# Performance work log

Measured on AMD Instinct MI355X. Metric: run time of the kernel, lower is better.

## Reference

```python
import jax, jax.numpy as jnp
import numpy as np

VOCAB = 10000
HIDDEN = 256
BATCH = 32
SEQ = 256


def setup_inputs() -> dict:
    key = jax.random.key(0)
    ks = jax.random.split(key, 7)
    s = 1.0 / np.sqrt(HIDDEN)  # torch nn.RNN/Linear init scale
    return {
        "inputs": jax.random.randint(ks[0], (BATCH, SEQ), 0, VOCAB),
        "state": jnp.zeros((1, BATCH, HIDDEN), dtype=jnp.float32),
        "W_ih": jax.random.uniform(ks[1], (HIDDEN, VOCAB), jnp.float32, -s, s),
        "b_ih": jax.random.uniform(ks[2], (HIDDEN,), jnp.float32, -s, s),
        "W_hh": jax.random.uniform(ks[3], (HIDDEN, HIDDEN), jnp.float32, -s, s),
        "b_hh": jax.random.uniform(ks[4], (HIDDEN,), jnp.float32, -s, s),
        "W_out": jax.random.uniform(ks[5], (VOCAB, HIDDEN), jnp.float32, -s, s),
        "b_out": jax.random.uniform(ks[6], (VOCAB,), jnp.float32, -s, s),
    }


def reference(inputs, state, W_ih, b_ih, W_hh, b_hh, W_out, b_out):
    # one_hot(inputs.T) @ W_ih.T is exactly a row-gather of W_ih.T (one-hot
    # entries are exactly 1.0), so gather gives bitwise-identical math.
    # xproj: (seq, batch, hidden)
    xproj = W_ih.T[inputs.T] + b_ih + b_hh

    def step(h, x_t):
        h = jnp.tanh(x_t + h @ W_hh.T)  # (batch, hidden)
        return h, h

    h_last, Y = jax.lax.scan(step, state[0], xproj)  # Y: (seq, batch, hidden)
    logits = Y.reshape(-1, HIDDEN) @ W_out.T + b_out  # (seq*batch, vocab)
    return logits, h_last[None]
```

## Files before the change

kernel.cpp:

```cpp
#include <hip/hip_runtime.h>

#define VOCAB 10000
#define HIDDEN 256
#define BATCH 32
#define SEQ 256
#define M_ROWS 8192
#define NPAD 10112
#define NTILES 79
#define MTILES 64
#define LOGITS_ELEMS 81920000LL

typedef __attribute__((ext_vector_type(8))) short short8;
typedef __attribute__((ext_vector_type(4))) float f32x4;

static __device__ __forceinline__ unsigned short f32_to_bf16(float f) {
    unsigned u = __float_as_uint(f);
    u += 0x7fffu + ((u >> 16) & 1u);
    return (unsigned short)(u >> 16);
}

__global__ __launch_bounds__(256) void transpose_wih(const float* __restrict__ W_ih,
                                                     float* __restrict__ W_ihT) {
    __shared__ float tile[64][65];
    const int v0   = (blockIdx.x >> 2) * 64;
    const int h0   = (blockIdx.x & 3) * 64;
    const int lane = threadIdx.x & 63;
    const int wv   = threadIdx.x >> 6;

#pragma unroll
    for (int i = 0; i < 16; ++i) {
        const int row = i * 4 + wv;
        const int v   = v0 + lane;
        if (v < VOCAB)
            tile[row][lane] = W_ih[(long)(h0 + row) * VOCAB + v];
    }
    __syncthreads();
#pragma unroll
    for (int i = 0; i < 16; ++i) {
        const int vrow = i * 4 + wv;
        const int v    = v0 + vrow;
        if (v < VOCAB)
            W_ihT[(long)v * HIDDEN + h0 + lane] = tile[lane][vrow];
    }
}

__global__ __launch_bounds__(256) void prep_wout(const float* __restrict__ W_out,
                                                 unsigned short* __restrict__ Wb) {
    const int n = blockIdx.x;
    const int k = threadIdx.x;
    float v = (n < VOCAB) ? W_out[(long)n * HIDDEN + k] : 0.f;
    Wb[(long)n * HIDDEN + k] = f32_to_bf16(v);
}

__global__ __launch_bounds__(512, 2) void scan_kernel(
        const int*   __restrict__ inputs,
        const float* __restrict__ state,
        const float* __restrict__ W_hh,
        const float* __restrict__ b_ih,
        const float* __restrict__ b_hh,
        const float* __restrict__ W_ihT,
        unsigned short* __restrict__ Ybf,
        float* __restrict__ hout)
{
    __shared__ float hbuf[HIDDEN];
    __shared__ float psum[4 * HIDDEN];

    const int b  = blockIdx.x;
    const int t  = threadIdx.x;
    const int jj = t & 63;
    const int q  = (t >> 6) & 3;
    const int h2 = t >> 8;

    float w[2][64];
#pragma unroll
    for (int r = 0; r < 2; ++r) {
        const float* src = W_hh + (jj + 64 * (2 * h2 + r)) * HIDDEN + 64 * q;
#pragma unroll
        for (int k4 = 0; k4 < 16; ++k4) {
            const float4 v = *(const float4*)(src + 4 * k4);
            w[r][4 * k4 + 0] = v.x;
            w[r][4 * k4 + 1] = v.y;
            w[r][4 * k4 + 2] = v.z;
            w[r][4 * k4 + 3] = v.w;
        }
    }

    float biasv = 0.f, xcur = 0.f;
    if (t < HIDDEN) {
        biasv   = b_ih[t] + b_hh[t];
        hbuf[t] = state[b * HIDDEN + t];
        const int tok0 = inputs[b * SEQ];
        xcur = W_ihT[(long)tok0 * HIDDEN + t];
    }
    __syncthreads();

    for (int step = 0; step < SEQ; ++step) {
        float xnext = 0.f;
        if (t < HIDDEN && step + 1 < SEQ) {
            const int tokn = inputs[b * SEQ + step + 1];
            xnext = W_ihT[(long)tokn * HIDDEN + t];
        }

        float a00 = 0.f, a01 = 0.f, a10 = 0.f, a11 = 0.f;
#pragma unroll
        for (int k4 = 0; k4 < 8; ++k4) {
            const float4 hv = *(const float4*)&hbuf[64 * q + 4 * k4];
            a00 = fmaf(w[0][4 * k4 + 0], hv.x, a00);
            a00 = fmaf(w[0][4 * k4 + 1], hv.y, a00);
            a00 = fmaf(w[0][4 * k4 + 2], hv.z, a00);
            a00 = fmaf(w[0][4 * k4 + 3], hv.w, a00);
            a10 = fmaf(w[1][4 * k4 + 0], hv.x, a10);
            a10 = fmaf(w[1][4 * k4 + 1], hv.y, a10);
            a10 = fmaf(w[1][4 * k4 + 2], hv.z, a10);
            a10 = fmaf(w[1][4 * k4 + 3], hv.w, a10);
        }
#pragma unroll
        for (int k4 = 8; k4 < 16; ++k4) {
            const float4 hv = *(const float4*)&hbuf[64 * q + 4 * k4];
            a01 = fmaf(w[0][4 * k4 + 0], hv.x, a01);
            a01 = fmaf(w[0][4 * k4 + 1], hv.y, a01);
            a01 = fmaf(w[0][4 * k4 + 2], hv.z, a01);
            a01 = fmaf(w[0][4 * k4 + 3], hv.w, a01);
            a11 = fmaf(w[1][4 * k4 + 0], hv.x, a11);
            a11 = fmaf(w[1][4 * k4 + 1], hv.y, a11);
            a11 = fmaf(w[1][4 * k4 + 2], hv.z, a11);
            a11 = fmaf(w[1][4 * k4 + 3], hv.w, a11);
        }
        psum[q * HIDDEN + jj + 64 * (2 * h2 + 0)] = a00 + a01;
        psum[q * HIDDEN + jj + 64 * (2 * h2 + 1)] = a10 + a11;
        __syncthreads();

        if (t < HIDDEN) {
            const float s = psum[t] + psum[HIDDEN + t]
                          + psum[2 * HIDDEN + t] + psum[3 * HIDDEN + t];
            const float hnew = tanhf(s + xcur + biasv);
            hbuf[t] = hnew;
            Ybf[((long)step * BATCH + b) * HIDDEN + t] = f32_to_bf16(hnew);
            xcur = xnext;
        }
        __syncthreads();
    }

    if (t < HIDDEN) hout[b * HIDDEN + t] = hbuf[t];
}

__global__ __launch_bounds__(256) void gemm_kernel(
        const unsigned short* __restrict__ A,
        const unsigned short* __restrict__ B,
        const float* __restrict__ bias,
        float* __restrict__ C)
{
    __shared__ unsigned short lA[128 * 64];
    __shared__ unsigned short lB[128 * 64];

    const int t     = threadIdx.x;
    const int bid   = blockIdx.x;
    const int ntile = bid % NTILES;
    const int mtile = bid / NTILES;
    const long m0   = (long)mtile * 128;
    const long n0   = (long)ntile * 128;
    const int lane  = t & 63;
    const int wave  = t >> 6;
    const int wm    = (wave & 1) * 64;
    const int wn    = (wave >> 1) * 64;
    const int l15   = lane & 15;
    const int quad  = lane >> 4;

    const f32x4 zero = {0.f, 0.f, 0.f, 0.f};
    f32x4 acc[4][4];
#pragma unroll
    for (int i = 0; i < 4; ++i)
#pragma unroll
        for (int j = 0; j < 4; ++j)
            acc[i][j] = zero;

    for (int kb = 0; kb < 4; ++kb) {
        if (kb) __syncthreads();
#pragma unroll
        for (int it = 0; it < 4; ++it) {
            const int c   = it * 256 + t;
            const int row = c >> 3;
            const int k8  = c & 7;
            const unsigned short* ga = A + (m0 + row) * HIDDEN + kb * 64 + k8 * 8;
            const unsigned short* gb = B + (n0 + row) * HIDDEN + kb * 64 + k8 * 8;
            __builtin_amdgcn_global_load_lds(
                (const __attribute__((address_space(1))) void*)ga,
                (__attribute__((address_space(3))) void*)(lA + c * 8), 16, 0, 0);
            __builtin_amdgcn_global_load_lds(
                (const __attribute__((address_space(1))) void*)gb,
                (__attribute__((address_space(3))) void*)(lB + c * 8), 16, 0, 0);
        }
        __syncthreads();

#pragma unroll
        for (int ki = 0; ki < 2; ++ki) {
            short8 af[4], bf[4];
#pragma unroll
            for (int i = 0; i < 4; ++i) {
                af[i] = *(const short8*)&lA[(wm + 16 * i + l15) * 64 + ki * 32 + quad * 8];
                bf[i] = *(const short8*)&lB[(wn + 16 * i + l15) * 64 + ki * 32 + quad * 8];
            }
#pragma unroll
            for (int i = 0; i < 4; ++i)
#pragma unroll
                for (int j = 0; j < 4; ++j)
                    acc[i][j] = __builtin_amdgcn_mfma_f32_16x16x32_bf16(
                        af[i], bf[j], acc[i][j], 0, 0, 0);
        }
    }

#pragma unroll
    for (int j = 0; j < 4; ++j) {
        const long col = n0 + wn + 16 * j + l15;
        if (col < VOCAB) {
            const float bv = bias[col];
#pragma unroll
            for (int i = 0; i < 4; ++i) {
                const long row = m0 + wm + 16 * i + quad * 4;
                float* Cp = C + row * VOCAB + col;
#pragma unroll
                for (int r = 0; r < 4; ++r)
                    Cp[(long)r * VOCAB] = acc[i][j][r] + bv;
            }
        }
    }
}

extern "C" void kernel_launch(void* const* d_in, const int* in_sizes, int n_in,
                              void* d_out, int out_size, void* d_ws, size_t ws_size,
                              hipStream_t stream) {
    const int*   inputs = (const int*)  d_in[0];
    const float* state  = (const float*)d_in[1];
    const float* W_ih   = (const float*)d_in[2];
    const float* b_ih   = (const float*)d_in[3];
    const float* W_hh   = (const float*)d_in[4];
    const float* b_hh   = (const float*)d_in[5];
    const float* W_out  = (const float*)d_in[6];
    const float* b_out  = (const float*)d_in[7];
    float* out = (float*)d_out;

    char* ws = (char*)d_ws;
    float*          W_ihT = (float*)ws;
    unsigned short* Wb    = (unsigned short*)(ws + 10240000);
    unsigned short* Ybf   = (unsigned short*)(ws + 15417344);

    transpose_wih<<<157 * 4, 256, 0, stream>>>(W_ih, W_ihT);
    prep_wout<<<NPAD, 256, 0, stream>>>(W_out, Wb);
    scan_kernel<<<BATCH, 512, 0, stream>>>(inputs, state, W_hh, b_ih, b_hh,
                                           W_ihT, Ybf, out + LOGITS_ELEMS);
    gemm_kernel<<<MTILES * NTILES, 256, 0, stream>>>(Ybf, Wb, b_out, out);
}
```

Measured before the change: 639.3 us.

## Fuse RNN scan and output GEMM into persistent cooperative kernel with progress flags

```diff
diff --git a/kernel.cpp b/kernel.cpp
--- a/kernel.cpp
+++ b/kernel.cpp
@@ -4,11 +4,14 @@
 #define HIDDEN 256
 #define BATCH 32
 #define SEQ 256
-#define M_ROWS 8192
 #define NPAD 10112
 #define NTILES 79
 #define MTILES 64
+#define TOTAL_TILES 5056
+#define CHUNK 4
+#define NCHUNKS 1264
 #define LOGITS_ELEMS 81920000LL
+#define GRID_BLOCKS 256
 
 typedef __attribute__((ext_vector_type(8))) short short8;
 typedef __attribute__((ext_vector_type(4))) float f32x4;
@@ -20,8 +23,10 @@
 }
 
 __global__ __launch_bounds__(256) void transpose_wih(const float* __restrict__ W_ih,
-                                                     float* __restrict__ W_ihT) {
+                                                     float* __restrict__ W_ihT,
+                                                     int* __restrict__ sync_ws) {
     __shared__ float tile[64][65];
+    if (blockIdx.x == 0 && threadIdx.x < 33) sync_ws[threadIdx.x] = 0;
     const int v0   = (blockIdx.x >> 2) * 64;
     const int h0   = (blockIdx.x & 3) * 64;
     const int lane = threadIdx.x & 63;
@@ -52,7 +57,7 @@
     Wb[(long)n * HIDDEN + k] = f32_to_bf16(v);
 }
 
-__global__ __launch_bounds__(512, 2) void scan_kernel(
+__global__ __launch_bounds__(512, 2) void fused_kernel(
         const int*   __restrict__ inputs,
         const float* __restrict__ state,
         const float* __restrict__ W_hh,
@@ -60,167 +65,214 @@
         const float* __restrict__ b_hh,
         const float* __restrict__ W_ihT,
         unsigned short* __restrict__ Ybf,
-        float* __restrict__ hout)
+        float* __restrict__ hout,
+        const unsigned short* __restrict__ Wb,
+        const float* __restrict__ b_out,
+        float* __restrict__ C,
+        int* __restrict__ prog,
+        int* __restrict__ disp)
 {
     __shared__ float hbuf[HIDDEN];
     __shared__ float psum[4 * HIDDEN];
-
-    const int b  = blockIdx.x;
-    const int t  = threadIdx.x;
-    const int jj = t & 63;
-    const int q  = (t >> 6) & 3;
-    const int h2 = t >> 8;
-
-    float w[2][64];
-#pragma unroll
-    for (int r = 0; r < 2; ++r) {
-        const float* src = W_hh + (jj + 64 * (2 * h2 + r)) * HIDDEN + 64 * q;
-#pragma unroll
-        for (int k4 = 0; k4 < 16; ++k4) {
-            const float4 v = *(const float4*)(src + 4 * k4);
-            w[r][4 * k4 + 0] = v.x;
-            w[r][4 * k4 + 1] = v.y;
-            w[r][4 * k4 + 2] = v.z;
-            w[r][4 * k4 + 3] = v.w;
-        }
-    }
-
-    float biasv = 0.f, xcur = 0.f;
-    if (t < HIDDEN) {
-        biasv   = b_ih[t] + b_hh[t];
-        hbuf[t] = state[b * HIDDEN + t];
-        const int tok0 = inputs[b * SEQ];
-        xcur = W_ihT[(long)tok0 * HIDDEN + t];
-    }
-    __syncthreads();
-
-    for (int step = 0; step < SEQ; ++step) {
-        float xnext = 0.f;
-        if (t < HIDDEN && step + 1 < SEQ) {
-            const int tokn = inputs[b * SEQ + step + 1];
-            xnext = W_ihT[(long)tokn * HIDDEN + t];
-        }
-
-        float a00 = 0.f, a01 = 0.f, a10 = 0.f, a11 = 0.f;
-#pragma unroll
-        for (int k4 = 0; k4 < 8; ++k4) {
-            const float4 hv = *(const float4*)&hbuf[64 * q + 4 * k4];
-            a00 = fmaf(w[0][4 * k4 + 0], hv.x, a00);
-            a00 = fmaf(w[0][4 * k4 + 1], hv.y, a00);
-            a00 = fmaf(w[0][4 * k4 + 2], hv.z, a00);
-            a00 = fmaf(w[0][4 * k4 + 3], hv.w, a00);
-            a10 = fmaf(w[1][4 * k4 + 0], hv.x, a10);
-            a10 = fmaf(w[1][4 * k4 + 1], hv.y, a10);
-            a10 = fmaf(w[1][4 * k4 + 2], hv.z, a10);
-            a10 = fmaf(w[1][4 * k4 + 3], hv.w, a10);
-        }
-#pragma unroll
-        for (int k4 = 8; k4 < 16; ++k4) {
-            const float4 hv = *(const float4*)&hbuf[64 * q + 4 * k4];
-            a01 = fmaf(w[0][4 * k4 + 0], hv.x, a01);
-            a01 = fmaf(w[0][4 * k4 + 1], hv.y, a01);
-            a01 = fmaf(w[0][4 * k4 + 2], hv.z, a01);
-            a01 = fmaf(w[0][4 * k4 + 3], hv.w, a01);
-            a11 = fmaf(w[1][4 * k4 + 0], hv.x, a11);
-            a11 = fmaf(w[1][4 * k4 + 1], hv.y, a11);
-            a11 = fmaf(w[1][4 * k4 + 2], hv.z, a11);
-            a11 = fmaf(w[1][4 * k4 + 3], hv.w, a11);
-        }
-        psum[q * HIDDEN + jj + 64 * (2 * h2 + 0)] = a00 + a01;
-        psum[q * HIDDEN + jj + 64 * (2 * h2 + 1)] = a10 + a11;
+    __shared__ __align__(16) unsigned short lA[2][128 * 64];
+    __shared__ __align__(16) unsigned short lB[2][128 * 64];
+    __shared__ int sh_g;
+    __shared__ char occ_pad[16384];
+
+    const int t = threadIdx.x;
+    if (disp == nullptr) occ_pad[0] = 1;
+
+    if (blockIdx.x < BATCH) {
+        const int b  = blockIdx.x;
+        const int jj = t & 63;
+        const int q  = (t >> 6) & 3;
+        const int h2 = t >> 8;
+
+        float w[2][64];
+#pragma unroll
+        for (int r = 0; r < 2; ++r) {
+            const float* src = W_hh + (jj + 64 * (2 * h2 + r)) * HIDDEN + 64 * q;
+#pragma unroll
+            for (int k4 = 0; k4 < 16; ++k4) {
+                const float4 v = *(const float4*)(src + 4 * k4);
+                w[r][4 * k4 + 0] = v.x;
+                w[r][4 * k4 + 1] = v.y;
+                w[r][4 * k4 + 2] = v.z;
+                w[r][4 * k4 + 3] = v.w;
+            }
+        }
+
+        float biasv = 0.f, xcur = 0.f;
+        if (t < HIDDEN) {
+            biasv   = b_ih[t] + b_hh[t];
+            hbuf[t] = state[b * HIDDEN + t];
+            const int tok0 = inputs[b * SEQ];
+            xcur = W_ihT[(long)tok0 * HIDDEN + t];
+        }
         __syncthreads();
 
-        if (t < HIDDEN) {
-            const float s = psum[t] + psum[HIDDEN + t]
-                          + psum[2 * HIDDEN + t] + psum[3 * HIDDEN + t];
-            const float hnew = tanhf(s + xcur + biasv);
-            hbuf[t] = hnew;
-            Ybf[((long)step * BATCH + b) * HIDDEN + t] = f32_to_bf16(hnew);
-            xcur = xnext;
-        }
+        for (int step = 0; step < SEQ; ++step) {
+            float xnext = 0.f;
+            if (t < HIDDEN && step + 1 < SEQ) {
+                const int tokn = inputs[b * SEQ + step + 1];
+                xnext = W_ihT[(long)tokn * HIDDEN + t];
+            }
+
+            float a00 = 0.f, a01 = 0.f, a10 = 0.f, a11 = 0.f;
+#pragma unroll
+            for (int k4 = 0; k4 < 8; ++k4) {
+                const float4 hv = *(const float4*)&hbuf[64 * q + 4 * k4];
+                a00 = fmaf(w[0][4 * k4 + 0], hv.x, a00);
+                a00 = fmaf(w[0][4 * k4 + 1], hv.y, a00);
+                a00 = fmaf(w[0][4 * k4 + 2], hv.z, a00);
+                a00 = fmaf(w[0][4 * k4 + 3], hv.w, a00);
+                a10 = fmaf(w[1][4 * k4 + 0], hv.x, a10);
+                a10 = fmaf(w[1][4 * k4 + 1], hv.y, a10);
+                a10 = fmaf(w[1][4 * k4 + 2], hv.z, a10);
+                a10 = fmaf(w[1][4 * k4 + 3], hv.w, a10);
+            }
+#pragma unroll
+            for (int k4 = 8; k4 < 16; ++k4) {
+                const float4 hv = *(const float4*)&hbuf[64 * q + 4 * k4];
+                a01 = fmaf(w[0][4 * k4 + 0], hv.x, a01);
+                a01 = fmaf(w[0][4 * k4 + 1], hv.y, a01);
+                a01 = fmaf(w[0][4 * k4 + 2], hv.z, a01);
+                a01 = fmaf(w[0][4 * k4 + 3], hv.w, a01);
+                a11 = fmaf(w[1][4 * k4 + 0], hv.x, a11);
+                a11 = fmaf(w[1][4 * k4 + 1], hv.y, a11);
+                a11 = fmaf(w[1][4 * k4 + 2], hv.z, a11);
+                a11 = fmaf(w[1][4 * k4 + 3], hv.w, a11);
+            }
+            psum[q * HIDDEN + jj + 64 * (2 * h2 + 0)] = a00 + a01;
+            psum[q * HIDDEN + jj + 64 * (2 * h2 + 1)] = a10 + a11;
+            __syncthreads();
+
+            if (t < HIDDEN) {
+                const float s = psum[t] + psum[HIDDEN + t]
+                              + psum[2 * HIDDEN + t] + psum[3 * HIDDEN + t];
+                const float hnew = tanhf(s + xcur + biasv);
+                hbuf[t] = hnew;
+                Ybf[((long)step * BATCH + b) * HIDDEN + t] = f32_to_bf16(hnew);
+                xcur = xnext;
+            }
+            __syncthreads();
+
+            if (((step & 3) == 3) && t == 0) {
+                __builtin_amdgcn_fence(__ATOMIC_RELEASE, "agent");
+                __hip_atomic_store(&prog[b], step + 1, __ATOMIC_RELAXED,
+                                   __HIP_MEMORY_SCOPE_AGENT);
+            }
+        }
+        if (t < HIDDEN) hout[b * HIDDEN + t] = hbuf[t];
         __syncthreads();
     }
 
-    if (t < HIDDEN) hout[b * HIDDEN + t] = hbuf[t];
-}
-
-__global__ __launch_bounds__(256) void gemm_kernel(
-        const unsigned short* __restrict__ A,
-        const unsigned short* __restrict__ B,
-        const float* __restrict__ bias,
-        float* __restrict__ C)
-{
-    __shared__ unsigned short lA[128 * 64];
-    __shared__ unsigned short lB[128 * 64];
-
-    const int t     = threadIdx.x;
-    const int bid   = blockIdx.x;
-    const int ntile = bid % NTILES;
-    const int mtile = bid / NTILES;
-    const long m0   = (long)mtile * 128;
-    const long n0   = (long)ntile * 128;
-    const int lane  = t & 63;
-    const int wave  = t >> 6;
-    const int wm    = (wave & 1) * 64;
-    const int wn    = (wave >> 1) * 64;
-    const int l15   = lane & 15;
-    const int quad  = lane >> 4;
-
+    const int lane = t & 63;
+    const int wave = t >> 6;
+    const int wm   = (wave & 1) * 64;
+    const int wn   = (wave >> 1) * 32;
+    const int l15  = lane & 15;
+    const int quad = lane >> 4;
     const f32x4 zero = {0.f, 0.f, 0.f, 0.f};
-    f32x4 acc[4][4];
-#pragma unroll
-    for (int i = 0; i < 4; ++i)
-#pragma unroll
-        for (int j = 0; j < 4; ++j)
-            acc[i][j] = zero;
-
-    for (int kb = 0; kb < 4; ++kb) {
-        if (kb) __syncthreads();
-#pragma unroll
-        for (int it = 0; it < 4; ++it) {
-            const int c   = it * 256 + t;
-            const int row = c >> 3;
-            const int k8  = c & 7;
-            const unsigned short* ga = A + (m0 + row) * HIDDEN + kb * 64 + k8 * 8;
-            const unsigned short* gb = B + (n0 + row) * HIDDEN + kb * 64 + k8 * 8;
-            __builtin_amdgcn_global_load_lds(
-                (const __attribute__((address_space(1))) void*)ga,
-                (__attribute__((address_space(3))) void*)(lA + c * 8), 16, 0, 0);
-            __builtin_amdgcn_global_load_lds(
-                (const __attribute__((address_space(1))) void*)gb,
-                (__attribute__((address_space(3))) void*)(lB + c * 8), 16, 0, 0);
-        }
+
+    for (;;) {
+        if (t == 0) sh_g = atomicAdd(disp, 1);
         __syncthreads();
-
-#pragma unroll
-        for (int ki = 0; ki < 2; ++ki) {
-            short8 af[4], bf[4];
-#pragma unroll
-            for (int i = 0; i < 4; ++i) {
-                af[i] = *(const short8*)&lA[(wm + 16 * i + l15) * 64 + ki * 32 + quad * 8];
-                bf[i] = *(const short8*)&lB[(wn + 16 * i + l15) * 64 + ki * 32 + quad * 8];
-            }
+        const int chunk = sh_g;
+        if (chunk >= NCHUNKS) break;
+
+        const int g0   = chunk * CHUNK;
+        const int need = 4 * ((g0 + CHUNK - 1) / NTILES) + 4;
+        if (t == 0) {
+            for (;;) {
+                bool ok = true;
+                for (int bb = 0; bb < BATCH; ++bb)
+                    ok &= (__hip_atomic_load(&prog[bb], __ATOMIC_RELAXED,
+                                             __HIP_MEMORY_SCOPE_AGENT) >= need);
+                if (ok) break;
+                __builtin_amdgcn_s_sleep(8);
+            }
+            __builtin_amdgcn_fence(__ATOMIC_ACQUIRE, "agent");
+        }
+        __syncthreads();
+
+        for (int g = g0; g < g0 + CHUNK; ++g) {
+            const int mt = g / NTILES;
+            const int nt = g - mt * NTILES;
+            const long m0 = (long)mt * 128;
+            const long n0 = (long)nt * 128;
+
+            f32x4 acc[4][2];
 #pragma unroll
             for (int i = 0; i < 4; ++i)
 #pragma unroll
-                for (int j = 0; j < 4; ++j)
-                    acc[i][j] = __builtin_amdgcn_mfma_f32_16x16x32_bf16(
-                        af[i], bf[j], acc[i][j], 0, 0, 0);
-        }
-    }
-
-#pragma unroll
-    for (int j = 0; j < 4; ++j) {
-        const long col = n0 + wn + 16 * j + l15;
-        if (col < VOCAB) {
-            const float bv = bias[col];
-#pragma unroll
-            for (int i = 0; i < 4; ++i) {
-                const long row = m0 + wm + 16 * i + quad * 4;
-                float* Cp = C + row * VOCAB + col;
-#pragma unroll
-                for (int r = 0; r < 4; ++r)
-                    Cp[(long)r * VOCAB] = acc[i][j][r] + bv;
+                for (int j = 0; j < 2; ++j)
+                    acc[i][j] = zero;
+
+            auto stage = [&](int kb, int buf) {
+#pragma unroll
+                for (int it = 0; it < 2; ++it) {
+                    const int c   = it * 512 + t;
+                    const int row = c >> 3;
+                    const int sk8 = (c & 7) ^ (row & 7);
+                    const unsigned short* ga = Ybf + (m0 + row) * HIDDEN + kb * 64 + sk8 * 8;
+                    const unsigned short* gb = Wb  + (n0 + row) * HIDDEN + kb * 64 + sk8 * 8;
+                    __builtin_amdgcn_global_load_lds(
+                        (const __attribute__((address_space(1))) void*)ga,
+                        (__attribute__((address_space(3))) void*)(&lA[buf][c * 8]), 16, 0, 0);
+                    __builtin_amdgcn_global_load_lds(
+                        (const __attribute__((address_space(1))) void*)gb,
+                        (__attribute__((address_space(3))) void*)(&lB[buf][c * 8]), 16, 0, 0);
+                }
+            };
+
+            stage(0, 0);
+            __syncthreads();
+#pragma unroll
+            for (int kb = 0; kb < 4; ++kb) {
+                if (kb < 3) stage(kb + 1, (kb + 1) & 1);
+                const unsigned short* bufA = lA[kb & 1];
+                const unsigned short* bufB = lB[kb & 1];
+#pragma unroll
+                for (int ki = 0; ki < 2; ++ki) {
+                    short8 af[4], bfr[2];
+#pragma unroll
+                    for (int i = 0; i < 4; ++i) {
+                        const int r = wm + 16 * i + l15;
+                        af[i] = *(const short8*)
+                            &bufA[r * 64 + (((ki * 4 + quad) ^ (r & 7)) * 8)];
+                    }
+#pragma unroll
+                    for (int j = 0; j < 2; ++j) {
+                        const int r = wn + 16 * j + l15;
+                        bfr[j] = *(const short8*)
+                            &bufB[r * 64 + (((ki * 4 + quad) ^ (r & 7)) * 8)];
+                    }
+#pragma unroll
+                    for (int i = 0; i < 4; ++i)
+#pragma unroll
+                        for (int j = 0; j < 2; ++j)
+                            acc[i][j] = __builtin_amdgcn_mfma_f32_16x16x32_bf16(
+                                af[i], bfr[j], acc[i][j], 0, 0, 0);
+                }
+                if (kb < 3) __syncthreads();
+            }
+
+#pragma unroll
+            for (int j = 0; j < 2; ++j) {
+                const long col = n0 + wn + 16 * j + l15;
+                if (col < VOCAB) {
+                    const float bv = b_out[col];
+#pragma unroll
+                    for (int i = 0; i < 4; ++i) {
+                        const long row = m0 + wm + 16 * i + quad * 4;
+                        float* Cp = C + row * VOCAB + col;
+#pragma unroll
+                        for (int r = 0; r < 4; ++r)
+                            __builtin_nontemporal_store(acc[i][j][r] + bv,
+                                                        Cp + (long)r * VOCAB);
+                    }
+                }
             }
         }
     }
@@ -243,10 +295,27 @@
     float*          W_ihT = (float*)ws;
     unsigned short* Wb    = (unsigned short*)(ws + 10240000);
     unsigned short* Ybf   = (unsigned short*)(ws + 15417344);
-
-    transpose_wih<<<157 * 4, 256, 0, stream>>>(W_ih, W_ihT);
+    int*            prog  = (int*)(ws + 19611648);
+    int*            disp  = prog + 32;
+    float*          hout  = out + LOGITS_ELEMS;
+
+    transpose_wih<<<157 * 4, 256, 0, stream>>>(W_ih, W_ihT, prog);
     prep_wout<<<NPAD, 256, 0, stream>>>(W_out, Wb);
-    scan_kernel<<<BATCH, 512, 0, stream>>>(inputs, state, W_hh, b_ih, b_hh,
-                                           W_ihT, Ybf, out + LOGITS_ELEMS);
-    gemm_kernel<<<MTILES * NTILES, 256, 0, stream>>>(Ybf, Wb, b_out, out);
-}
+
+    void* args[13];
+    args[0]  = (void*)&inputs;
+    args[1]  = (void*)&state;
+    args[2]  = (void*)&W_hh;
+    args[3]  = (void*)&b_ih;
+    args[4]  = (void*)&b_hh;
+    args[5]  = (void*)&W_ihT;
+    args[6]  = (void*)&Ybf;
+    args[7]  = (void*)&hout;
+    args[8]  = (void*)&Wb;
+    args[9]  = (void*)&b_out;
+    args[10] = (void*)&out;
+    args[11] = (void*)&prog;
+    args[12] = (void*)&disp;
+    hipLaunchCooperativeKernel((void*)fused_kernel, dim3(GRID_BLOCKS), dim3(512),
+                               args, 0, stream);
+}
```

Result: slower. 717.6 us (+12.3%).

## Double-buffer GEMM LDS tiles, XOR-swizzle layout, and use nontemporal output stores

Applied to the files above, without the earlier changes.

```diff
diff --git a/kernel.cpp b/kernel.cpp
--- a/kernel.cpp
+++ b/kernel.cpp
@@ -4,7 +4,6 @@
 #define HIDDEN 256
 #define BATCH 32
 #define SEQ 256
-#define M_ROWS 8192
 #define NPAD 10112
 #define NTILES 79
 #define MTILES 64
@@ -150,8 +149,8 @@
         const float* __restrict__ bias,
         float* __restrict__ C)
 {
-    __shared__ unsigned short lA[128 * 64];
-    __shared__ unsigned short lB[128 * 64];
+    __shared__ __align__(16) unsigned short lA[2][128 * 64];
+    __shared__ __align__(16) unsigned short lB[2][128 * 64];
 
     const int t     = threadIdx.x;
     const int bid   = blockIdx.x;
@@ -174,31 +173,42 @@
         for (int j = 0; j < 4; ++j)
             acc[i][j] = zero;
 
-    for (int kb = 0; kb < 4; ++kb) {
-        if (kb) __syncthreads();
+    auto stage = [&](int kb, int buf) {
 #pragma unroll
         for (int it = 0; it < 4; ++it) {
             const int c   = it * 256 + t;
             const int row = c >> 3;
-            const int k8  = c & 7;
-            const unsigned short* ga = A + (m0 + row) * HIDDEN + kb * 64 + k8 * 8;
-            const unsigned short* gb = B + (n0 + row) * HIDDEN + kb * 64 + k8 * 8;
+            const int sk8 = (c & 7) ^ (row & 7);
+            const unsigned short* ga = A + (m0 + row) * HIDDEN + kb * 64 + sk8 * 8;
+            const unsigned short* gb = B + (n0 + row) * HIDDEN + kb * 64 + sk8 * 8;
             __builtin_amdgcn_global_load_lds(
                 (const __attribute__((address_space(1))) void*)ga,
-                (__attribute__((address_space(3))) void*)(lA + c * 8), 16, 0, 0);
+                (__attribute__((address_space(3))) void*)(&lA[buf][c * 8]), 16, 0, 0);
             __builtin_amdgcn_global_load_lds(
                 (const __attribute__((address_space(1))) void*)gb,
-                (__attribute__((address_space(3))) void*)(lB + c * 8), 16, 0, 0);
-        }
-        __syncthreads();
-
+                (__attribute__((address_space(3))) void*)(&lB[buf][c * 8]), 16, 0, 0);
+        }
+    };
+
+    stage(0, 0);
+    __syncthreads();
+
+#pragma unroll
+    for (int kb = 0; kb < 4; ++kb) {
+        if (kb < 3) stage(kb + 1, (kb + 1) & 1);
+        const unsigned short* bufA = lA[kb & 1];
+        const unsigned short* bufB = lB[kb & 1];
 #pragma unroll
         for (int ki = 0; ki < 2; ++ki) {
             short8 af[4], bf[4];
 #pragma unroll
             for (int i = 0; i < 4; ++i) {
-                af[i] = *(const short8*)&lA[(wm + 16 * i + l15) * 64 + ki * 32 + quad * 8];
-                bf[i] = *(const short8*)&lB[(wn + 16 * i + l15) * 64 + ki * 32 + quad * 8];
+                const int ra = wm + 16 * i + l15;
+                af[i] = *(const short8*)
+                    &bufA[ra * 64 + (((ki * 4 + quad) ^ (ra & 7)) * 8)];
+                const int rb = wn + 16 * i + l15;
+                bf[i] = *(const short8*)
+                    &bufB[rb * 64 + (((ki * 4 + quad) ^ (rb & 7)) * 8)];
             }
 #pragma unroll
             for (int i = 0; i < 4; ++i)
@@ -207,6 +217,7 @@
                     acc[i][j] = __builtin_amdgcn_mfma_f32_16x16x32_bf16(
                         af[i], bf[j], acc[i][j], 0, 0, 0);
         }
+        if (kb < 3) __syncthreads();
     }
 
 #pragma unroll
@@ -220,7 +231,8 @@
                 float* Cp = C + row * VOCAB + col;
 #pragma unroll
                 for (int r = 0; r < 4; ++r)
-                    Cp[(long)r * VOCAB] = acc[i][j][r] + bv;
+                    __builtin_nontemporal_store(acc[i][j][r] + bv,
+                                                Cp + (long)r * VOCAB);
             }
         }
     }
```

Result: faster. 603.5 us (-5.6%).
